# Performance work log

Hardware: AMD Instinct MI355X
Metric: run time of the kernel (lower is better)

## Reference

```python
import jax, jax.numpy as jnp
import numpy as np

B, T, C, H = 2, 2048, 1024, 16
HD = C // H  # 64

def setup_inputs() -> dict:
    key = jax.random.key(0)
    ks = jax.random.split(key, 9)
    s = 0.02
    return {
        "x": jax.random.normal(ks[0], (B, T, C), jnp.float32),
        "Wq": jax.random.normal(ks[1], (C, C), jnp.float32) * s,
        "bq": jax.random.normal(ks[2], (C,), jnp.float32) * s,
        "Wk": jax.random.normal(ks[3], (C, C), jnp.float32) * s,
        "bk": jax.random.normal(ks[4], (C,), jnp.float32) * s,
        "Wv": jax.random.normal(ks[5], (C, C), jnp.float32) * s,
        "bv": jax.random.normal(ks[6], (C,), jnp.float32) * s,
        "Wp": jax.random.normal(ks[7], (C, C), jnp.float32) * s,
        "bp": jax.random.normal(ks[8], (C,), jnp.float32) * s,
    }

def reference(x, Wq, bq, Wk, bk, Wv, bv, Wp, bp):
    Bb, Tt, Cc = x.shape
    hd = Cc // H
    # project and split heads: [B, H, T, hd]
    def heads(W, b):
        return (x @ W.T + b).reshape(Bb, Tt, H, hd).transpose(0, 2, 1, 3)
    q, k, v = heads(Wq, bq), heads(Wk, bk), heads(Wv, bv)
    scale = 1.0 / np.sqrt(hd).astype(np.float32)
    att = jnp.einsum('bhqd,bhkd->bhqk', q, k) * scale
    causal = jnp.tril(jnp.ones((Tt, Tt), bool))
    att = jnp.where(causal[None, None], att, -jnp.inf)
    att = jax.nn.softmax(att, axis=-1)
    y = jnp.einsum('bhqk,bhkd->bhqd', att, v)
    y = y.transpose(0, 2, 1, 3).reshape(Bb, Tt, Cc)
    return y @ Wp.T + bp
```

## Files before the change

### kernel.cpp

```cpp
#include <hip/hip_runtime.h>
#include <hip/hip_bf16.h>

#define Tsz 2048
#define Csz 1024
#define Hn 16

typedef short s8v __attribute__((ext_vector_type(8)));
typedef short s4v __attribute__((ext_vector_type(4)));
typedef float f4v __attribute__((ext_vector_type(4)));

#define QSCALE (0.125f * 1.44269504088896f)

__device__ __forceinline__ unsigned short bfr(float x) {
    return (unsigned short)((__builtin_bit_cast(unsigned, x) + 0x8000u) >> 16);
}
__device__ __forceinline__ unsigned pack2_rn(float a, float b) {
    const unsigned ua = __builtin_bit_cast(unsigned, a) + 0x8000u;
    const unsigned ub = __builtin_bit_cast(unsigned, b) + 0x8000u;
    return (ua >> 16) | (ub & 0xFFFF0000u);
}

__device__ __forceinline__ void gload_lds(const void* g, void* l) {
    __builtin_amdgcn_global_load_lds(
        (const __attribute__((address_space(1))) void*)g,
        (__attribute__((address_space(3))) void*)l, 16, 0, 0);
}

__global__ void cvt6(const float* __restrict__ x, const float* __restrict__ wq,
                     const float* __restrict__ wk, const float* __restrict__ wv,
                     const float* __restrict__ wp,
                     short* __restrict__ xo, short* __restrict__ qo,
                     short* __restrict__ ko, short* __restrict__ vo,
                     short* __restrict__ po) {
    const int bx = blockIdx.x;
    const float* in; short* out; int ib;
    if (bx < 4096) { in = x; out = xo; ib = bx; }
    else {
        const int r = bx - 4096, w = r >> 10;
        ib = r & 1023;
        switch (w) {
            case 0: in = wq; out = qo; break;
            case 1: in = wk; out = ko; break;
            case 2: in = wv; out = vo; break;
            default: in = wp; out = po; break;
        }
    }
    const int i = ib * 1024 + threadIdx.x * 4;
    float4 v = *(const float4*)(in + i);
    int2 o;
    o.x = (int)pack2_rn(v.x, v.y);
    o.y = (int)pack2_rn(v.z, v.w);
    *(int2*)(out + i) = o;
}

__global__ __launch_bounds__(256, 3) void qkv_gemm(
    const short* __restrict__ X,
    const short* __restrict__ Wq, const short* __restrict__ Wk, const short* __restrict__ Wv,
    const float* __restrict__ bq, const float* __restrict__ bk, const float* __restrict__ bv,
    short* __restrict__ Qo, short* __restrict__ Ko, short* __restrict__ Vto)
{
    const int z = blockIdx.z;
    const short* W = (z == 0) ? Wq : (z == 1) ? Wk : Wv;
    const float* bias = (z == 0) ? bq : (z == 1) ? bk : bv;

    __shared__ __align__(16) short Ash[128 * 32];
    __shared__ __align__(16) short Bsh[128 * 32];
    __shared__ __align__(16) short TR[64 * 72];

    const int tid = threadIdx.x, lane = tid & 63, wave = tid >> 6;
    const int ln = lane & 15, hi = lane >> 4;
    const int m0 = blockIdx.x * 128, n0 = blockIdx.y * 128;
    const int wm = (wave >> 1) * 64, wn = (wave & 1) * 64;

    const short* Ag = X + (size_t)(m0 + (tid >> 2)) * Csz + (tid & 3) * 8;
    const short* Bg = W + (size_t)(n0 + (tid >> 2)) * Csz + (tid & 3) * 8;

    f4v acc[4][4];
    #pragma unroll
    for (int mt = 0; mt < 4; mt++)
        #pragma unroll
        for (int nt = 0; nt < 4; nt++)
            #pragma unroll
            for (int i = 0; i < 4; i++) acc[mt][nt][i] = 0.f;

    for (int k0 = 0; k0 < Csz; k0 += 32) {
        __syncthreads();
        gload_lds(Ag + k0, Ash + tid * 8);
        gload_lds(Ag + k0 + (size_t)64 * Csz, Ash + 2048 + tid * 8);
        gload_lds(Bg + k0, Bsh + tid * 8);
        gload_lds(Bg + k0 + (size_t)64 * Csz, Bsh + 2048 + tid * 8);
        __syncthreads();

        s8v af[4], bfr_[4];
        #pragma unroll
        for (int mt = 0; mt < 4; mt++)
            af[mt] = *(const s8v*)(Ash + (wm + mt * 16 + ln) * 32 + hi * 8);
        #pragma unroll
        for (int nt = 0; nt < 4; nt++)
            bfr_[nt] = *(const s8v*)(Bsh + (wn + nt * 16 + ln) * 32 + hi * 8);
        #pragma unroll
        for (int mt = 0; mt < 4; mt++)
            #pragma unroll
            for (int nt = 0; nt < 4; nt++)
                acc[mt][nt] = __builtin_amdgcn_mfma_f32_16x16x32_bf16(af[mt], bfr_[nt], acc[mt][nt], 0, 0, 0);
    }

    if (z == 2) {
        const int b = m0 >> 11, t0 = m0 & 2047;
        float bvv[4];
        #pragma unroll
        for (int nt = 0; nt < 4; nt++) bvv[nt] = bias[n0 + wn + nt * 16 + ln];
        #pragma unroll
        for (int ph = 0; ph < 4; ph++) {
            const int mh = ph >> 1, nh = ph & 1;
            __syncthreads();
            if ((wave >> 1) == mh && (wave & 1) == nh) {
                #pragma unroll
                for (int mt = 0; mt < 4; mt++)
                    #pragma unroll
                    for (int nt = 0; nt < 4; nt++) {
                        int2 pk;
                        pk.x = (int)pack2_rn(acc[mt][nt][0] + bvv[nt], acc[mt][nt][1] + bvv[nt]);
                        pk.y = (int)pack2_rn(acc[mt][nt][2] + bvv[nt], acc[mt][nt][3] + bvv[nt]);
                        *(int2*)(TR + (nt * 16 + ln) * 72 + mt * 16 + hi * 4) = pk;
                    }
            }
            __syncthreads();
            const int chl = tid >> 2, seg = tid & 3;
            const s8v r0 = *(const s8v*)(TR + chl * 72 + seg * 16);
            const s8v r1 = *(const s8v*)(TR + chl * 72 + seg * 16 + 8);
            short* dst = Vto + (size_t)(b * 1024 + n0 + nh * 64 + chl) * Tsz + t0 + mh * 64 + seg * 16;
            *(s8v*)(dst) = r0;
            *(s8v*)(dst + 8) = r1;
        }
        return;
    }

    const float scale = (z == 0) ? QSCALE : 1.0f;
    short* out = (z == 0) ? Qo : Ko;

    #pragma unroll
    for (int nt = 0; nt < 4; nt++) {
        const int col = n0 + wn + nt * 16 + ln;
        const float bvv = bias[col];
        #pragma unroll
        for (int mt = 0; mt < 4; mt++) {
            const int row0 = m0 + wm + mt * 16 + hi * 4;
            #pragma unroll
            for (int i = 0; i < 4; i++)
                out[(size_t)(row0 + i) * Csz + col] = (short)bfr((acc[mt][nt][i] + bvv) * scale);
        }
    }
}

__global__ __launch_bounds__(256, 2) void proj_gemm(
    const short* __restrict__ A, const short* __restrict__ W,
    const float* __restrict__ bias, float* __restrict__ out)
{
    __shared__ __align__(16) short Ash[128 * 32];
    __shared__ __align__(16) short Bsh[64 * 32];

    const int tid = threadIdx.x, lane = tid & 63, wave = tid >> 6;
    const int ln = lane & 15, hi = lane >> 4;
    const int m0 = blockIdx.x * 128, n0 = blockIdx.y * 64;
    const int wm = (wave >> 1) * 64, wn = (wave & 1) * 32;

    const short* Ag = A + (size_t)(m0 + (tid >> 2)) * Csz + (tid & 3) * 8;
    const short* Bg = W + (size_t)(n0 + (tid >> 2)) * Csz + (tid & 3) * 8;

    f4v acc[4][2];
    #pragma unroll
    for (int mt = 0; mt < 4; mt++)
        #pragma unroll
        for (int nt = 0; nt < 2; nt++)
            #pragma unroll
            for (int i = 0; i < 4; i++) acc[mt][nt][i] = 0.f;

    for (int k0 = 0; k0 < Csz; k0 += 32) {
        __syncthreads();
        gload_lds(Ag + k0, Ash + tid * 8);
        gload_lds(Ag + k0 + (size_t)64 * Csz, Ash + 2048 + tid * 8);
        gload_lds(Bg + k0, Bsh + tid * 8);
        __syncthreads();

        s8v af[4], bfr_[2];
        #pragma unroll
        for (int mt = 0; mt < 4; mt++)
            af[mt] = *(const s8v*)(Ash + (wm + mt * 16 + ln) * 32 + hi * 8);
        #pragma unroll
        for (int nt = 0; nt < 2; nt++)
            bfr_[nt] = *(const s8v*)(Bsh + (wn + nt * 16 + ln) * 32 + hi * 8);
        #pragma unroll
        for (int mt = 0; mt < 4; mt++)
            #pragma unroll
            for (int nt = 0; nt < 2; nt++)
                acc[mt][nt] = __builtin_amdgcn_mfma_f32_16x16x32_bf16(af[mt], bfr_[nt], acc[mt][nt], 0, 0, 0);
    }

    #pragma unroll
    for (int nt = 0; nt < 2; nt++) {
        const int col = n0 + wn + nt * 16 + ln;
        const float bvv = bias[col];
        #pragma unroll
        for (int mt = 0; mt < 4; mt++)
            #pragma unroll
            for (int i = 0; i < 4; i++)
                out[(size_t)(m0 + wm + mt * 16 + hi * 4 + i) * Csz + col] = acc[mt][nt][i] + bvv;
    }
}

__global__ __launch_bounds__(512, 2) void attn9(
    const short* __restrict__ Q, const short* __restrict__ Kg,
    const short* __restrict__ Vt, short* __restrict__ Y)
{
    __shared__ __align__(16) short Ksh[2][64 * 72];
    __shared__ __align__(16) short Vsh[2][64 * 72];
    __shared__ __align__(16) short Psh[8][16 * 72];

    const int tid = threadIdx.x, lane = tid & 63, wave = tid >> 6;
    const int wv = wave & 3, g = wave >> 2;
    const int ln = lane & 15, hi = lane >> 4;
    const int p = blockIdx.x;
    const int qts[2] = { g ? 15 - p : p, g ? 16 + p : 31 - p };
    const int bh = blockIdx.y;
    const size_t base = (size_t)(bh >> 4) * Tsz * Csz + (size_t)(bh & 15) * 64;
    const size_t vtbase = (size_t)bh * 64 * Tsz;
    const int qrel = wv * 16 + ln;
    short* Pq = Psh[wave];

    s8v qf[2][2];
    #pragma unroll
    for (int t = 0; t < 2; t++)
        #pragma unroll
        for (int kk = 0; kk < 2; kk++)
            qf[t][kk] = *(const s8v*)(Q + base + (size_t)(qts[t] * 64 + qrel) * Csz + kk * 32 + hi * 8);

    f4v o[2][4];
    float lsum[2] = {0.f, 0.f};
    #pragma unroll
    for (int t = 0; t < 2; t++)
        #pragma unroll
        for (int dt = 0; dt < 4; dt++)
            #pragma unroll
            for (int i = 0; i < 4; i++) o[t][dt][i] = 0.f;

    const int sr = tid >> 3, sc = (tid & 7) * 8;
    const short* Kp = Kg + base + (size_t)sr * Csz + sc;
    const short* Vp = Vt + vtbase + (size_t)sr * Tsz + sc;
    const int swo = sr * 72 + sc;

    const int nkb = 32 - p;

    s8v kR = *(const s8v*)(Kp);
    s8v vR = *(const s8v*)(Vp);
    *(s8v*)(&Ksh[0][swo]) = kR;
    *(s8v*)(&Vsh[0][swo]) = vR;
    kR = *(const s8v*)(Kp + (size_t)64 * Csz);
    vR = *(const s8v*)(Vp + 64);
    __syncthreads();

    for (int kb = 0; kb < nkb; kb++) {
        const int buf = kb & 1;
        if (kb + 1 < nkb) {
            *(s8v*)(&Ksh[buf ^ 1][swo]) = kR;
            *(s8v*)(&Vsh[buf ^ 1][swo]) = vR;
            const int knx = (kb + 2 < nkb) ? (kb + 2) * 64 : (nkb - 1) * 64;
            kR = *(const s8v*)(Kp + (size_t)knx * Csz);
            vR = *(const s8v*)(Vp + knx);
        }

        s8v kf[2][4], vf[2][4];
        #pragma unroll
        for (int nt = 0; nt < 4; nt++)
            #pragma unroll
            for (int kk = 0; kk < 2; kk++) {
                kf[kk][nt] = *(const s8v*)(&Ksh[buf][(nt * 16 + ln) * 72 + kk * 32 + hi * 8]);
                vf[kk][nt] = *(const s8v*)(&Vsh[buf][(nt * 16 + ln) * 72 + kk * 32 + hi * 8]);
            }

        #pragma unroll
        for (int t = 0; t < 2; t++) {
            if (kb > qts[t]) continue;
            const bool dg = (kb == qts[t]);

            f4v s[4];
            #pragma unroll
            for (int nt = 0; nt < 4; nt++) {
                #pragma unroll
                for (int i = 0; i < 4; i++) s[nt][i] = 0.f;
                s[nt] = __builtin_amdgcn_mfma_f32_16x16x32_bf16(kf[0][nt], qf[t][0], s[nt], 0, 0, 0);
                s[nt] = __builtin_amdgcn_mfma_f32_16x16x32_bf16(kf[1][nt], qf[t][1], s[nt], 0, 0, 0);
            }

            #pragma unroll
            for (int nt = 0; nt < 4; nt++) {
                float pv[4];
                #pragma unroll
                for (int i = 0; i < 4; i++) pv[i] = exp2f(s[nt][i]);
                if (dg) {
                    const int kr = nt * 16 + hi * 4;
                    #pragma unroll
                    for (int i = 0; i < 4; i++)
                        if (kr + i > qrel) pv[i] = 0.f;
                }
                lsum[t] += (pv[0] + pv[1]) + (pv[2] + pv[3]);
                int2 w;
                w.x = (int)pack2_rn(pv[0], pv[1]);
                w.y = (int)pack2_rn(pv[2], pv[3]);
                *(int2*)(Pq + ln * 72 + nt * 16 + hi * 4) = w;
            }
            const s8v pb0 = *(const s8v*)(Pq + ln * 72 + hi * 8);
            const s8v pb1 = *(const s8v*)(Pq + ln * 72 + 32 + hi * 8);

            #pragma unroll
            for (int dt = 0; dt < 4; dt++) {
                o[t][dt] = __builtin_amdgcn_mfma_f32_16x16x32_bf16(vf[0][dt], pb0, o[t][dt], 0, 0, 0);
                o[t][dt] = __builtin_amdgcn_mfma_f32_16x16x32_bf16(vf[1][dt], pb1, o[t][dt], 0, 0, 0);
            }
        }
        __syncthreads();
    }

    #pragma unroll
    for (int t = 0; t < 2; t++) {
        float l = lsum[t];
        l += __shfl_xor(l, 16);
        l += __shfl_xor(l, 32);
        const float inv = 1.0f / l;
        const int qrow = qts[t] * 64 + qrel;
        #pragma unroll
        for (int dt = 0; dt < 4; dt++) {
            int2 w;
            w.x = (int)pack2_rn(o[t][dt][0] * inv, o[t][dt][1] * inv);
            w.y = (int)pack2_rn(o[t][dt][2] * inv, o[t][dt][3] * inv);
            *(int2*)(Y + base + (size_t)qrow * Csz + dt * 16 + hi * 4) = w;
        }
    }
}

extern "C" void kernel_launch(void* const* d_in, const int* in_sizes, int n_in,
                              void* d_out, int out_size, void* d_ws, size_t ws_size,
                              hipStream_t stream) {
    const float* x  = (const float*)d_in[0];
    const float* Wq = (const float*)d_in[1];
    const float* bq = (const float*)d_in[2];
    const float* Wk = (const float*)d_in[3];
    const float* bk = (const float*)d_in[4];
    const float* Wv = (const float*)d_in[5];
    const float* bv = (const float*)d_in[6];
    const float* Wp = (const float*)d_in[7];
    const float* bp = (const float*)d_in[8];

    char* ws = (char*)d_ws;
    short* Xb  = (short*)(ws);
    short* Wqb = (short*)(ws + (8u  << 20));
    short* Wkb = (short*)(ws + (10u << 20));
    short* Wvb = (short*)(ws + (12u << 20));
    short* Wpb = (short*)(ws + (14u << 20));
    short* Qb  = (short*)(ws + (16u << 20));
    short* Kb  = (short*)(ws + (24u << 20));
    short* Vtb = (short*)(ws + (32u << 20));
    short* Yb  = (short*)(ws + (40u << 20));

    hipLaunchKernelGGL(cvt6, dim3(8192), dim3(256), 0, stream,
                       x, Wq, Wk, Wv, Wp, Xb, Wqb, Wkb, Wvb, Wpb);

    hipLaunchKernelGGL(qkv_gemm, dim3(32, 8, 3), dim3(256), 0, stream,
                       Xb, Wqb, Wkb, Wvb, bq, bk, bv, Qb, Kb, Vtb);

    hipLaunchKernelGGL(attn9, dim3(8, 32), dim3(512), 0, stream, Qb, Kb, Vtb, Yb);

    hipLaunchKernelGGL(proj_gemm, dim3(32, 16), dim3(256), 0, stream, Yb, Wpb, bp, (float*)d_out);
}
```

Measured before the change: 191.7 us.

## Split attention into one query tile per block with single-buffered K/V

The attention kernel now gives each 256-thread block a single 64-row query tile, where before each 512-thread block handled two paired tiles. The launch becomes a flat grid of 1024 blocks, and the block index is remapped so that heavy and light causal tiles alternate to balance load. K/V staging goes from a double-buffered LDS ring to a single buffer filled from registers between two barriers. This is meant to add parallelism and occupancy, but it adds an extra barrier per key block, reuses each K/V tile across fewer query rows, and gives up the paired-tile balance inside a block.

```diff
diff --git a/kernel.cpp b/kernel.cpp
--- a/kernel.cpp
+++ b/kernel.cpp
@@ -209,64 +209,64 @@
     }
 }
 
-__global__ __launch_bounds__(512, 2) void attn9(
+__global__ __launch_bounds__(256, 4) void attn10(
     const short* __restrict__ Q, const short* __restrict__ Kg,
     const short* __restrict__ Vt, short* __restrict__ Y)
 {
-    __shared__ __align__(16) short Ksh[2][64 * 72];
-    __shared__ __align__(16) short Vsh[2][64 * 72];
-    __shared__ __align__(16) short Psh[8][16 * 72];
+    __shared__ __align__(16) short Ksh[64 * 72];
+    __shared__ __align__(16) short Vsh[64 * 72];
+    __shared__ __align__(16) short Psh[4][16 * 72];
 
     const int tid = threadIdx.x, lane = tid & 63, wave = tid >> 6;
-    const int wv = wave & 3, g = wave >> 2;
     const int ln = lane & 15, hi = lane >> 4;
-    const int p = blockIdx.x;
-    const int qts[2] = { g ? 15 - p : p, g ? 16 + p : 31 - p };
-    const int bh = blockIdx.y;
+
+    const int n = blockIdx.x;
+    const int c = n & 255, j = n >> 8;
+    const int bh = (j << 3) | (c >> 5);
+    const int t = c & 31;
+    const int qt = (j & 1) ? t : 31 - t;
+
     const size_t base = (size_t)(bh >> 4) * Tsz * Csz + (size_t)(bh & 15) * 64;
     const size_t vtbase = (size_t)bh * 64 * Tsz;
-    const int qrel = wv * 16 + ln;
+    const int qrel = wave * 16 + ln;
     short* Pq = Psh[wave];
 
-    s8v qf[2][2];
-    #pragma unroll
-    for (int t = 0; t < 2; t++)
-        #pragma unroll
-        for (int kk = 0; kk < 2; kk++)
-            qf[t][kk] = *(const s8v*)(Q + base + (size_t)(qts[t] * 64 + qrel) * Csz + kk * 32 + hi * 8);
-
-    f4v o[2][4];
-    float lsum[2] = {0.f, 0.f};
-    #pragma unroll
-    for (int t = 0; t < 2; t++)
-        #pragma unroll
-        for (int dt = 0; dt < 4; dt++)
-            #pragma unroll
-            for (int i = 0; i < 4; i++) o[t][dt][i] = 0.f;
+    s8v qf[2];
+    #pragma unroll
+    for (int kk = 0; kk < 2; kk++)
+        qf[kk] = *(const s8v*)(Q + base + (size_t)(qt * 64 + qrel) * Csz + kk * 32 + hi * 8);
+
+    f4v o[4];
+    float lsum = 0.f;
+    #pragma unroll
+    for (int dt = 0; dt < 4; dt++)
+        #pragma unroll
+        for (int i = 0; i < 4; i++) o[dt][i] = 0.f;
 
     const int sr = tid >> 3, sc = (tid & 7) * 8;
     const short* Kp = Kg + base + (size_t)sr * Csz + sc;
     const short* Vp = Vt + vtbase + (size_t)sr * Tsz + sc;
     const int swo = sr * 72 + sc;
-
-    const int nkb = 32 - p;
-
-    s8v kR = *(const s8v*)(Kp);
-    s8v vR = *(const s8v*)(Vp);
-    *(s8v*)(&Ksh[0][swo]) = kR;
-    *(s8v*)(&Vsh[0][swo]) = vR;
-    kR = *(const s8v*)(Kp + (size_t)64 * Csz);
-    vR = *(const s8v*)(Vp + 64);
+    const int nkb = qt + 1;
+
+    s8v k0 = *(const s8v*)(Kp);
+    s8v k1 = *(const s8v*)(Kp + (size_t)32 * Csz);
+    s8v v0 = *(const s8v*)(Vp);
+    s8v v1 = *(const s8v*)(Vp + (size_t)32 * Tsz);
+    *(s8v*)(&Ksh[swo]) = k0;
+    *(s8v*)(&Ksh[swo + 32 * 72]) = k1;
+    *(s8v*)(&Vsh[swo]) = v0;
+    *(s8v*)(&Vsh[swo + 32 * 72]) = v1;
     __syncthreads();
 
     for (int kb = 0; kb < nkb; kb++) {
-        const int buf = kb & 1;
-        if (kb + 1 < nkb) {
-            *(s8v*)(&Ksh[buf ^ 1][swo]) = kR;
-            *(s8v*)(&Vsh[buf ^ 1][swo]) = vR;
-            const int knx = (kb + 2 < nkb) ? (kb + 2) * 64 : (nkb - 1) * 64;
-            kR = *(const s8v*)(Kp + (size_t)knx * Csz);
-            vR = *(const s8v*)(Vp + knx);
+        const bool more = (kb + 1 < nkb);
+        if (more) {
+            const size_t ko = (size_t)(kb + 1) * 64;
+            k0 = *(const s8v*)(Kp + ko * Csz);
+            k1 = *(const s8v*)(Kp + (ko + 32) * Csz);
+            v0 = *(const s8v*)(Vp + ko);
+            v1 = *(const s8v*)(Vp + ko + (size_t)32 * Tsz);
         }
 
         s8v kf[2][4], vf[2][4];
@@ -274,67 +274,67 @@
         for (int nt = 0; nt < 4; nt++)
             #pragma unroll
             for (int kk = 0; kk < 2; kk++) {
-                kf[kk][nt] = *(const s8v*)(&Ksh[buf][(nt * 16 + ln) * 72 + kk * 32 + hi * 8]);
-                vf[kk][nt] = *(const s8v*)(&Vsh[buf][(nt * 16 + ln) * 72 + kk * 32 + hi * 8]);
+                kf[kk][nt] = *(const s8v*)(&Ksh[(nt * 16 + ln) * 72 + kk * 32 + hi * 8]);
+                vf[kk][nt] = *(const s8v*)(&Vsh[(nt * 16 + ln) * 72 + kk * 32 + hi * 8]);
             }
 
-        #pragma unroll
-        for (int t = 0; t < 2; t++) {
-            if (kb > qts[t]) continue;
-            const bool dg = (kb == qts[t]);
-
-            f4v s[4];
-            #pragma unroll
-            for (int nt = 0; nt < 4; nt++) {
+        f4v s[4];
+        #pragma unroll
+        for (int nt = 0; nt < 4; nt++) {
+            #pragma unroll
+            for (int i = 0; i < 4; i++) s[nt][i] = 0.f;
+            s[nt] = __builtin_amdgcn_mfma_f32_16x16x32_bf16(kf[0][nt], qf[0], s[nt], 0, 0, 0);
+            s[nt] = __builtin_amdgcn_mfma_f32_16x16x32_bf16(kf[1][nt], qf[1], s[nt], 0, 0, 0);
+        }
+
+        const bool dg = !more;
+        #pragma unroll
+        for (int nt = 0; nt < 4; nt++) {
+            float pv[4];
+            #pragma unroll
+            for (int i = 0; i < 4; i++) pv[i] = exp2f(s[nt][i]);
+            if (dg) {
+                const int kr = nt * 16 + hi * 4;
                 #pragma unroll
-                for (int i = 0; i < 4; i++) s[nt][i] = 0.f;
-                s[nt] = __builtin_amdgcn_mfma_f32_16x16x32_bf16(kf[0][nt], qf[t][0], s[nt], 0, 0, 0);
-                s[nt] = __builtin_amdgcn_mfma_f32_16x16x32_bf16(kf[1][nt], qf[t][1], s[nt], 0, 0, 0);
+                for (int i = 0; i < 4; i++)
+                    if (kr + i > qrel) pv[i] = 0.f;
             }
-
-            #pragma unroll
-            for (int nt = 0; nt < 4; nt++) {
-                float pv[4];
-                #pragma unroll
-                for (int i = 0; i < 4; i++) pv[i] = exp2f(s[nt][i]);
-                if (dg) {
-                    const int kr = nt * 16 + hi * 4;
-                    #pragma unroll
-                    for (int i = 0; i < 4; i++)
-                        if (kr + i > qrel) pv[i] = 0.f;
-                }
-                lsum[t] += (pv[0] + pv[1]) + (pv[2] + pv[3]);
-                int2 w;
-                w.x = (int)pack2_rn(pv[0], pv[1]);
-                w.y = (int)pack2_rn(pv[2], pv[3]);
-                *(int2*)(Pq + ln * 72 + nt * 16 + hi * 4) = w;
-            }
-            const s8v pb0 = *(const s8v*)(Pq + ln * 72 + hi * 8);
-            const s8v pb1 = *(const s8v*)(Pq + ln * 72 + 32 + hi * 8);
-
-            #pragma unroll
-            for (int dt = 0; dt < 4; dt++) {
-                o[t][dt] = __builtin_amdgcn_mfma_f32_16x16x32_bf16(vf[0][dt], pb0, o[t][dt], 0, 0, 0);
-                o[t][dt] = __builtin_amdgcn_mfma_f32_16x16x32_bf16(vf[1][dt], pb1, o[t][dt], 0, 0, 0);
-            }
-        }
-        __syncthreads();
-    }
-
-    #pragma unroll
-    for (int t = 0; t < 2; t++) {
-        float l = lsum[t];
-        l += __shfl_xor(l, 16);
-        l += __shfl_xor(l, 32);
-        const float inv = 1.0f / l;
-        const int qrow = qts[t] * 64 + qrel;
+            lsum += (pv[0] + pv[1]) + (pv[2] + pv[3]);
+            int2 w;
+            w.x = (int)pack2_rn(pv[0], pv[1]);
+            w.y = (int)pack2_rn(pv[2], pv[3]);
+            *(int2*)(Pq + ln * 72 + nt * 16 + hi * 4) = w;
+        }
+        const s8v pb0 = *(const s8v*)(Pq + ln * 72 + hi * 8);
+        const s8v pb1 = *(const s8v*)(Pq + ln * 72 + 32 + hi * 8);
+
         #pragma unroll
         for (int dt = 0; dt < 4; dt++) {
-            int2 w;
-            w.x = (int)pack2_rn(o[t][dt][0] * inv, o[t][dt][1] * inv);
-            w.y = (int)pack2_rn(o[t][dt][2] * inv, o[t][dt][3] * inv);
-            *(int2*)(Y + base + (size_t)qrow * Csz + dt * 16 + hi * 4) = w;
-        }
+            o[dt] = __builtin_amdgcn_mfma_f32_16x16x32_bf16(vf[0][dt], pb0, o[dt], 0, 0, 0);
+            o[dt] = __builtin_amdgcn_mfma_f32_16x16x32_bf16(vf[1][dt], pb1, o[dt], 0, 0, 0);
+        }
+
+        if (more) {
+            __syncthreads();
+            *(s8v*)(&Ksh[swo]) = k0;
+            *(s8v*)(&Ksh[swo + 32 * 72]) = k1;
+            *(s8v*)(&Vsh[swo]) = v0;
+            *(s8v*)(&Vsh[swo + 32 * 72]) = v1;
+            __syncthreads();
+        }
+    }
+
+    float l = lsum;
+    l += __shfl_xor(l, 16);
+    l += __shfl_xor(l, 32);
+    const float inv = 1.0f / l;
+    const int qrow = qt * 64 + qrel;
+    #pragma unroll
+    for (int dt = 0; dt < 4; dt++) {
+        int2 w;
+        w.x = (int)pack2_rn(o[dt][0] * inv, o[dt][1] * inv);
+        w.y = (int)pack2_rn(o[dt][2] * inv, o[dt][3] * inv);
+        *(int2*)(Y + base + (size_t)qrow * Csz + dt * 16 + hi * 4) = w;
     }
 }
 
@@ -368,7 +368,7 @@
     hipLaunchKernelGGL(qkv_gemm, dim3(32, 8, 3), dim3(256), 0, stream,
                        Xb, Wqb, Wkb, Wvb, bq, bk, bv, Qb, Kb, Vtb);
 
-    hipLaunchKernelGGL(attn9, dim3(8, 32), dim3(512), 0, stream, Qb, Kb, Vtb, Yb);
+    hipLaunchKernelGGL(attn10, dim3(1024), dim3(256), 0, stream, Qb, Kb, Vtb, Yb);
 
     hipLaunchKernelGGL(proj_gemm, dim3(32, 16), dim3(256), 0, stream, Yb, Wpb, bp, (float*)d_out);
 }
```

Result: no change. 191.0 us (-0.4%).
